# Kernel tuning notes

Hardware: AMD Instinct MI355X
Metric: run time of the kernel (lower is better)

Reference implementation:

```python
import jax, jax.numpy as jnp
import numpy as np

DIM = 192
HEADS = 6

def conv1x1(x, w):
    # x: [b,c,h,w], w: [out,in]
    return jnp.einsum('oi,bihw->bohw', w, x)

def dwconv3x3(x, w):
    # x: [b,c,h,w], w: [c,1,3,3] depthwise
    return jax.lax.conv_general_dilated(
        x, w, window_strides=(1, 1), padding='SAME',
        dimension_numbers=('NCHW', 'OIHW', 'NCHW'),
        feature_group_count=x.shape[1])

def l2norm(x, eps=1e-12):
    n = jnp.sqrt(jnp.sum(x * x, axis=-1, keepdims=True))
    return x / jnp.maximum(n, eps)

def setup_inputs() -> dict:
    key = jax.random.key(0)
    ks = jax.random.split(key, 9)
    b, c, h, w = 8, DIM, 128, 128
    s = 1.0 / np.sqrt(c)
    return {
        'x': jax.random.normal(ks[0], (b, c, h, w), jnp.float32),
        'Wq': jax.random.normal(ks[1], (c, c), jnp.float32) * s,
        'Wk': jax.random.normal(ks[2], (c, c), jnp.float32) * s,
        'Wv': jax.random.normal(ks[3], (c, c), jnp.float32) * s,
        'Wq_dw': jax.random.normal(ks[4], (c, 1, 3, 3), jnp.float32) * (1.0 / 3.0),
        'Wk_dw': jax.random.normal(ks[5], (c, 1, 3, 3), jnp.float32) * (1.0 / 3.0),
        'Wv_dw': jax.random.normal(ks[6], (c, 1, 3, 3), jnp.float32) * (1.0 / 3.0),
        'rescale': jnp.ones((HEADS, 1, 1), jnp.float32),
        'Wp': jax.random.normal(ks[7], (c, c), jnp.float32) * s,
    }

def reference(x, Wq, Wk, Wv, Wq_dw, Wk_dw, Wv_dw, rescale, Wp):
    b, c, h, w = x.shape
    hd = c // HEADS  # per-head channels
    q = dwconv3x3(conv1x1(x, Wq), Wq_dw).reshape(b, HEADS, hd, h * w)
    k = dwconv3x3(conv1x1(x, Wk), Wk_dw).reshape(b, HEADS, hd, h * w)
    v = dwconv3x3(conv1x1(x, Wv), Wv_dw).reshape(b, HEADS, hd, h * w)
    q = l2norm(q)
    k = l2norm(k)
    # attn: [b, heads, hd, hd] -- small channel-wise attention
    attn = jnp.einsum('bhcn,bhdn->bhcd', q, k) * rescale
    attn = jax.nn.softmax(attn, axis=-1)
    out = jnp.einsum('bhcd,bhdn->bhcn', attn, v).reshape(b, c, h, w)
    return conv1x1(out, Wp)
```

## Files before the change

kernel.cpp:

```cpp
#include <hip/hip_runtime.h>
#include <hip/hip_bf16.h>


using bf16x8 = __attribute__((ext_vector_type(8))) short;
using f32x4  = __attribute__((ext_vector_type(4))) float;
using fvec4  = __attribute__((ext_vector_type(4))) float;

#define NB     8
#define CDIM   192
#define NHEADS 6
#define IMGW   128
#define NPIX   16384

__device__ __forceinline__ float b2f(unsigned short u){
  return __uint_as_float(((unsigned int)u) << 16);
}
__device__ __forceinline__ unsigned short f2b(float f){
  unsigned int x = __float_as_uint(f);
  return (unsigned short)((x + 0x7FFFu + ((x >> 16) & 1u)) >> 16);
}
__device__ __forceinline__ float ldT(const void* p, size_t i, int isbf){
  return isbf ? b2f(((const unsigned short*)p)[i]) : ((const float*)p)[i];
}
__device__ __forceinline__ f32x4 MF(bf16x8 a, bf16x8 b, f32x4 c){
  return __builtin_amdgcn_mfma_f32_16x16x32_bf16(a, b, c, 0, 0, 0);
}

__global__ void k_detect(const unsigned short* x, int* flag){
  int l = threadIdx.x;
  int cnt = 0;
#pragma unroll
  for (int i = 0; i < 2; ++i){
    unsigned short u = x[(l*2 + i)*2];
    float a = fabsf(b2f(u));
    if (a == 0.f || (a > 1e-4f && a < 20.f)) ++cnt;
  }
  int tot = __popcll(__ballot(cnt >= 1)) + __popcll(__ballot(cnt >= 2));
  if (l == 0) *flag = (tot > 64) ? 1 : 0;
}

__global__ __launch_bounds__(256) void k_prep(const void* Wq, const void* Wk, const void* Wv,
    unsigned short* Wqkv, const int* flag){
  int i = blockIdx.x*256 + threadIdx.x;
  if (i >= 576*192) return;
  int isbf = *flag;
  int m = i / 192, kk = i % 192;
  int t = m / 192;
  const void* W = (t == 0) ? Wq : (t == 1) ? Wk : Wv;
  Wqkv[i] = f2b(ldT(W, (size_t)(m % 192)*192 + kk, isbf));
}

__global__ __launch_bounds__(256) void k_conv1(const void* x, const unsigned short* Wqkv,
    unsigned short* q0, unsigned short* k0, unsigned short* v0, const int* flag){
  __shared__ unsigned short Bt[64][200];
  int tid = threadIdx.x;
  int nt = blockIdx.x, b = blockIdx.y;
  int n0 = nt * 64;
  int isbf = *flag;
  if (isbf){
    const unsigned short* xs = (const unsigned short*)x;
    for (int r = tid; r < 1536; r += 256){
      int k = r >> 3, j8 = (r & 7) * 8;
      bf16x8 v = *(const bf16x8*)(xs + (size_t)(b*CDIM + k)*NPIX + n0 + j8);
#pragma unroll
      for (int i = 0; i < 8; ++i) Bt[j8+i][k] = (unsigned short)v[i];
    }
  } else {
    const float* xf = (const float*)x;
    for (int r = tid; r < 3072; r += 256){
      int k = r >> 4, j4 = (r & 15) * 4;
      fvec4 v = *(const fvec4*)(xf + (size_t)(b*CDIM + k)*NPIX + n0 + j4);
#pragma unroll
      for (int i = 0; i < 4; ++i) Bt[j4+i][k] = f2b(v[i]);
    }
  }
  __syncthreads();
  int w = tid >> 6, l = tid & 63, lr = l & 15, lk = l >> 4;
#pragma unroll 1
  for (int t = 0; t < 3; ++t){
    f32x4 acc[3][4] = {};
    for (int kc = 0; kc < 6; ++kc){
      bf16x8 af[3];
#pragma unroll
      for (int g = 0; g < 3; ++g)
        af[g] = *(const bf16x8*)(Wqkv + ((size_t)t*CDIM + g*64 + w*16 + lr)*CDIM + kc*32 + lk*8);
#pragma unroll
      for (int nf = 0; nf < 4; ++nf){
        bf16x8 bfv = *(const bf16x8*)(&Bt[nf*16 + lr][kc*32 + lk*8]);
#pragma unroll
        for (int g = 0; g < 3; ++g) acc[g][nf] = MF(af[g], bfv, acc[g][nf]);
      }
    }
    unsigned short* dst = (t == 0) ? q0 : (t == 1) ? k0 : v0;
#pragma unroll
    for (int g = 0; g < 3; ++g)
#pragma unroll
      for (int nf = 0; nf < 4; ++nf)
#pragma unroll
        for (int r = 0; r < 4; ++r){
          int m = g*64 + w*16 + lk*4 + r;
          dst[(size_t)(b*CDIM + m)*NPIX + n0 + nf*16 + lr] = f2b(acc[g][nf][r]);
        }
  }
}

__global__ __launch_bounds__(256) void k_dw(unsigned short* q0, unsigned short* k0,
    unsigned short* v0, const void* wqd, const void* wkd, const void* wvd,
    float* Nsq, const int* flag){
  __shared__ unsigned short img[128][136];
  __shared__ float wred[4];
  int tid = threadIdx.x;
  int t = blockIdx.x, c = blockIdx.y, b = blockIdx.z;
  int isbf = *flag;
  unsigned short* base = ((t == 0) ? q0 : (t == 1) ? k0 : v0) + (size_t)(b*CDIM + c)*NPIX;
  const void* wd = (t == 0) ? wqd : (t == 1) ? wkd : wvd;
  float w9[9];
#pragma unroll
  for (int e = 0; e < 9; ++e) w9[e] = ldT(wd, (size_t)c*9 + e, isbf);
  for (int r = tid; r < 2048; r += 256){
    int row = r >> 4, col8 = (r & 15)*8;
    *(bf16x8*)(&img[row][col8]) = *(const bf16x8*)(base + row*IMGW + col8);
  }
  __syncthreads();
  int tr = tid >> 2, tc = tid & 3;
  int c0 = tc * 32, r0 = tr * 2;
  const bf16x8 zv = {0,0,0,0,0,0,0,0};
  int  rowi[4]; bool valid[4];
  bf16x8 cur[4], nxt[4];
  float carry[4];
#pragma unroll
  for (int d = 0; d < 4; ++d){
    rowi[d] = r0 - 1 + d;
    valid[d] = (rowi[d] >= 0) && (rowi[d] < 128);
    cur[d] = valid[d] ? *(const bf16x8*)(&img[rowi[d]][c0]) : zv;
    carry[d] = (valid[d] && c0 > 0) ? b2f(img[rowi[d]][c0 - 1]) : 0.f;
  }
  float sq = 0.f;
#pragma unroll
  for (int j = 0; j < 4; ++j){
    float right0[4];
    if (j < 3){
#pragma unroll
      for (int d = 0; d < 4; ++d){
        nxt[d] = valid[d] ? *(const bf16x8*)(&img[rowi[d]][c0 + 8*(j+1)]) : zv;
        right0[d] = b2f((unsigned short)nxt[d][0]);
      }
    } else {
#pragma unroll
      for (int d = 0; d < 4; ++d)
        right0[d] = (valid[d] && (c0 + 32 < 128)) ? b2f(img[rowi[d]][c0 + 32]) : 0.f;
    }
    float f[4][8];
#pragma unroll
    for (int d = 0; d < 4; ++d)
#pragma unroll
      for (int i = 0; i < 8; ++i) f[d][i] = b2f((unsigned short)cur[d][i]);
#pragma unroll
    for (int rr = 0; rr < 2; ++rr){
      float o[8];
#pragma unroll
      for (int cc = 0; cc < 8; ++cc){
        float a = 0.f;
#pragma unroll
        for (int d2 = 0; d2 < 3; ++d2){
          int d = rr + d2;
          float lf = (cc == 0) ? carry[d] : f[d][cc-1];
          float md = f[d][cc];
          float rt = (cc == 7) ? right0[d] : f[d][cc+1];
          a = fmaf(w9[d2*3+0], lf, a);
          a = fmaf(w9[d2*3+1], md, a);
          a = fmaf(w9[d2*3+2], rt, a);
        }
        o[cc] = a;
        if (t < 2) sq = fmaf(a, a, sq);
      }
      bf16x8 ov;
#pragma unroll
      for (int cc = 0; cc < 8; ++cc) ov[cc] = (short)f2b(o[cc]);
      *(bf16x8*)(base + (r0 + rr)*IMGW + c0 + 8*j) = ov;
    }
#pragma unroll
    for (int d = 0; d < 4; ++d) carry[d] = f[d][7];
    if (j < 3){
#pragma unroll
      for (int d = 0; d < 4; ++d) cur[d] = nxt[d];
    }
  }
  if (t < 2){
#pragma unroll
    for (int off = 32; off > 0; off >>= 1) sq += __shfl_xor(sq, off);
    if ((tid & 63) == 0) wred[tid >> 6] = sq;
    __syncthreads();
    if (tid == 0) Nsq[((size_t)b*2 + t)*CDIM + c] = wred[0] + wred[1] + wred[2] + wred[3];
  }
}

__global__ __launch_bounds__(256) void k_gram(const unsigned short* qd,
    const unsigned short* kd, float* Spart){
  __shared__ float S_lds[1024];
  int tid = threadIdx.x;
  int cs = blockIdx.x, h = blockIdx.y, b = blockIdx.z;
  int w = tid >> 6, l = tid & 63, lr = l & 15, lk = l >> 4;
  for (int e = tid; e < 1024; e += 256) S_lds[e] = 0.f;
  __syncthreads();
  const unsigned short* qb = qd + (size_t)(b*CDIM + h*32)*NPIX;
  const unsigned short* kb = kd + (size_t)(b*CDIM + h*32)*NPIX;
  f32x4 g4[2][2] = {};
  int pxb = cs*2048 + w*512 + lk*8;
#pragma unroll
  for (int kc = 0; kc < 16; ++kc){
    int px = pxb + kc*32;
    bf16x8 a0 = *(const bf16x8*)(qb + (size_t)lr*NPIX + px);
    bf16x8 a1 = *(const bf16x8*)(qb + (size_t)(16+lr)*NPIX + px);
    bf16x8 b0 = *(const bf16x8*)(kb + (size_t)lr*NPIX + px);
    bf16x8 b1 = *(const bf16x8*)(kb + (size_t)(16+lr)*NPIX + px);
    g4[0][0] = MF(a0, b0, g4[0][0]);
    g4[0][1] = MF(a0, b1, g4[0][1]);
    g4[1][0] = MF(a1, b0, g4[1][0]);
    g4[1][1] = MF(a1, b1, g4[1][1]);
  }
  for (int wv = 0; wv < 4; ++wv){
    if (w == wv){
#pragma unroll
      for (int mi = 0; mi < 2; ++mi)
#pragma unroll
        for (int ni = 0; ni < 2; ++ni)
#pragma unroll
          for (int r = 0; r < 4; ++r)
            S_lds[(mi*16 + lk*4 + r)*32 + ni*16 + lr] += g4[mi][ni][r];
    }
    __syncthreads();
  }
  int bidx = (b*NHEADS + h)*8 + cs;
  for (int e = tid; e < 1024; e += 256) Spart[(size_t)bidx*1024 + e] = S_lds[e];
}

__global__ __launch_bounds__(256) void k_attn(const float* Spart, const float* Nsq,
    const void* rescale, float* attnG, const int* flag){
  __shared__ float S[1024];
  __shared__ float rn[64];
  int bh = blockIdx.x, tid = threadIdx.x;
  int b = bh / NHEADS, h = bh % NHEADS;
  int isbf = *flag;
  for (int e = tid; e < 1024; e += 256){
    float a = 0.f;
    for (int st = 0; st < 8; ++st) a += Spart[((size_t)bh*8 + st)*1024 + e];
    S[e] = a;
  }
  if (tid < 64){
    int t = tid >> 5, ch = h*32 + (tid & 31);
    float a = Nsq[((size_t)b*2 + t)*CDIM + ch];
    rn[tid] = 1.f / fmaxf(sqrtf(a), 1e-12f);
  }
  __syncthreads();
  if (tid < 32){
    float sc = ldT(rescale, h, isbf);
    float lo[32], mx = -1e30f;
#pragma unroll
    for (int d = 0; d < 32; ++d){
      lo[d] = S[tid*32 + d] * rn[tid] * rn[32 + d] * sc;
      mx = fmaxf(mx, lo[d]);
    }
    float sum = 0.f;
#pragma unroll
    for (int d = 0; d < 32; ++d){ lo[d] = __expf(lo[d] - mx); sum += lo[d]; }
    float inv = 1.f / sum;
#pragma unroll
    for (int d = 0; d < 32; ++d) attnG[(size_t)bh*1024 + tid*32 + d] = lo[d] * inv;
  }
}

__global__ __launch_bounds__(256) void k_mmat(const void* Wp, const float* attnG,
    unsigned short* Mb, const int* flag){
  __shared__ float at[NHEADS*1024];
  __shared__ float wp[32][200];
  int b = blockIdx.x, og = blockIdx.y, tid = threadIdx.x;
  int isbf = *flag;
  for (int e = tid; e < NHEADS*1024; e += 256) at[e] = attnG[(size_t)b*NHEADS*1024 + e];
  for (int e = tid; e < 32*192; e += 256){
    int r = e / 192, cdx = e % 192;
    wp[r][cdx] = ldT(Wp, (size_t)(og*32 + r)*CDIM + cdx, isbf);
  }
  __syncthreads();
  int r = tid >> 3, cg = tid & 7;
#pragma unroll 1
  for (int i = 0; i < 24; ++i){
    int dg = cg*24 + i;
    int hh = dg >> 5, d = dg & 31;
    float a = 0.f;
#pragma unroll
    for (int cc = 0; cc < 32; ++cc)
      a += wp[r][hh*32 + cc] * at[hh*1024 + cc*32 + d];
    Mb[(size_t)b*CDIM*CDIM + (size_t)(og*32 + r)*CDIM + dg] = f2b(a);
  }
}

__global__ __launch_bounds__(256) void k_out(const unsigned short* v, const unsigned short* Mb,
    void* out, const int* flag){
  __shared__ unsigned short Bt[64][200];
  int tid = threadIdx.x;
  int nt = blockIdx.x, b = blockIdx.y;
  int n0 = nt * 64;
  for (int r = tid; r < 1536; r += 256){
    int k = r >> 3, j8 = (r & 7) * 8;
    bf16x8 vv = *(const bf16x8*)(v + (size_t)(b*CDIM + k)*NPIX + n0 + j8);
#pragma unroll
    for (int i = 0; i < 8; ++i) Bt[j8+i][k] = (unsigned short)vv[i];
  }
  __syncthreads();
  int w = tid >> 6, l = tid & 63, lr = l & 15, lk = l >> 4;
  const unsigned short* A = Mb + (size_t)b*CDIM*CDIM;
  f32x4 acc[3][4] = {};
  for (int kc = 0; kc < 6; ++kc){
    bf16x8 af[3];
#pragma unroll
    for (int g = 0; g < 3; ++g)
      af[g] = *(const bf16x8*)(A + (size_t)(g*64 + w*16 + lr)*CDIM + kc*32 + lk*8);
#pragma unroll
    for (int nf = 0; nf < 4; ++nf){
      bf16x8 bfv = *(const bf16x8*)(&Bt[nf*16 + lr][kc*32 + lk*8]);
#pragma unroll
      for (int g = 0; g < 3; ++g) acc[g][nf] = MF(af[g], bfv, acc[g][nf]);
    }
  }
  int isbf = *flag;
#pragma unroll
  for (int g = 0; g < 3; ++g)
#pragma unroll
    for (int nf = 0; nf < 4; ++nf)
#pragma unroll
      for (int r = 0; r < 4; ++r){
        int m = g*64 + w*16 + lk*4 + r;
        size_t oi = (size_t)(b*CDIM + m)*NPIX + n0 + nf*16 + lr;
        if (isbf) ((unsigned short*)out)[oi] = f2b(acc[g][nf][r]);
        else      ((float*)out)[oi] = acc[g][nf][r];
      }
}

extern "C" void kernel_launch(void* const* d_in, const int* in_sizes, int n_in,
                              void* d_out, int out_size, void* d_ws, size_t ws_size,
                              hipStream_t stream){
  const void* x   = d_in[0];
  const void* Wq  = d_in[1];
  const void* Wk  = d_in[2];
  const void* Wv  = d_in[3];
  const void* Wqd = d_in[4];
  const void* Wkd = d_in[5];
  const void* Wvd = d_in[6];
  const void* rsc = d_in[7];
  const void* Wp  = d_in[8];

  char* ws = (char*)d_ws;
  size_t o = 0;
  int* flag             = (int*)(ws + o);            o += 256;
  unsigned short* Wqkv  = (unsigned short*)(ws + o); o += (size_t)576*192*2;
  unsigned short* q0    = (unsigned short*)(ws + o); o += (size_t)NB*CDIM*NPIX*2;
  unsigned short* k0    = (unsigned short*)(ws + o); o += (size_t)NB*CDIM*NPIX*2;
  unsigned short* v0    = (unsigned short*)(ws + o); o += (size_t)NB*CDIM*NPIX*2;
  float* Spart          = (float*)(ws + o);          o += (size_t)384*1024*4;
  float* Nsq            = (float*)(ws + o);          o += (size_t)NB*2*CDIM*4;
  float* attnG          = (float*)(ws + o);          o += (size_t)48*1024*4;
  unsigned short* Mb    = (unsigned short*)(ws + o); o += (size_t)NB*CDIM*CDIM*2;

  k_detect<<<dim3(1), 64, 0, stream>>>((const unsigned short*)x, flag);
  k_prep  <<<dim3(432), 256, 0, stream>>>(Wq, Wk, Wv, Wqkv, flag);
  k_conv1 <<<dim3(256, 8), 256, 0, stream>>>(x, Wqkv, q0, k0, v0, flag);
  k_dw    <<<dim3(3, CDIM, NB), 256, 0, stream>>>(q0, k0, v0, Wqd, Wkd, Wvd, Nsq, flag);
  k_gram  <<<dim3(8, NHEADS, NB), 256, 0, stream>>>(q0, k0, Spart);
  k_attn  <<<dim3(48), 256, 0, stream>>>(Spart, Nsq, rsc, attnG, flag);
  k_mmat  <<<dim3(NB, 6), 256, 0, stream>>>(Wp, attnG, Mb, flag);
  k_out   <<<dim3(256, 8), 256, 0, stream>>>(v0, Mb, d_out, flag);
}
```

Baseline: 280.7 us.

## Split 1x1 conv into transpose pass plus register-resident GEMM over transposed x

Adds a separate kernel that transposes x into a pixel-major bf16 buffer, so the 1x1 conv kernel can load activation fragments straight from global memory into registers with no LDS staging. Each wave keeps its 32-pixel slice in registers and loops over all 576 output channels, streaming weight fragments and writing vectorized 4-element outputs. This removes the shared-memory transpose and the scattered scalar stores. In exchange it adds a full extra read and write of x, and the transpose kernel uses strided per-channel loads with only 32x8 blocks.

```diff
diff --git a/kernel.cpp b/kernel.cpp
--- a/kernel.cpp
+++ b/kernel.cpp
@@ -5,6 +5,7 @@
 using bf16x8 = __attribute__((ext_vector_type(8))) short;
 using f32x4  = __attribute__((ext_vector_type(4))) float;
 using fvec4  = __attribute__((ext_vector_type(4))) float;
+using u16x4  = __attribute__((ext_vector_type(4))) unsigned short;
 
 #define NB     8
 #define CDIM   192
@@ -50,57 +51,72 @@
   Wqkv[i] = f2b(ldT(W, (size_t)(m % 192)*192 + kk, isbf));
 }
 
-__global__ __launch_bounds__(256) void k_conv1(const void* x, const unsigned short* Wqkv,
-    unsigned short* q0, unsigned short* k0, unsigned short* v0, const int* flag){
-  __shared__ unsigned short Bt[64][200];
+__global__ __launch_bounds__(256) void k_xT(const void* x, unsigned short* xT, const int* flag){
+  int np = blockIdx.x*256 + threadIdx.x;
+  int b = blockIdx.y;
+  int n = np*2;
+  int isbf = *flag;
+  unsigned short* dst = xT + ((size_t)b*NPIX + n)*CDIM;
+#pragma unroll 1
+  for (int cg = 0; cg < 24; ++cg){
+    bf16x8 a0, a1;
+    if (isbf){
+      const unsigned short* xs = (const unsigned short*)x + (size_t)b*CDIM*NPIX;
+#pragma unroll
+      for (int i = 0; i < 8; ++i){
+        unsigned int u = *(const unsigned int*)(xs + (size_t)(cg*8+i)*NPIX + n);
+        a0[i] = (short)(u & 0xffffu);
+        a1[i] = (short)(u >> 16);
+      }
+    } else {
+      const float* xf = (const float*)x + (size_t)b*CDIM*NPIX;
+#pragma unroll
+      for (int i = 0; i < 8; ++i){
+        fvec4 dummy;
+        float f0 = xf[(size_t)(cg*8+i)*NPIX + n];
+        float f1 = xf[(size_t)(cg*8+i)*NPIX + n + 1];
+        a0[i] = (short)f2b(f0);
+        a1[i] = (short)f2b(f1);
+        (void)dummy;
+      }
+    }
+    *(bf16x8*)(dst + cg*8)        = a0;
+    *(bf16x8*)(dst + CDIM + cg*8) = a1;
+  }
+}
+
+__global__ __launch_bounds__(256) void k_conv1t(const unsigned short* xT,
+    const unsigned short* Wqkv, unsigned short* q0, unsigned short* k0,
+    unsigned short* v0){
   int tid = threadIdx.x;
-  int nt = blockIdx.x, b = blockIdx.y;
-  int n0 = nt * 64;
-  int isbf = *flag;
-  if (isbf){
-    const unsigned short* xs = (const unsigned short*)x;
-    for (int r = tid; r < 1536; r += 256){
-      int k = r >> 3, j8 = (r & 7) * 8;
-      bf16x8 v = *(const bf16x8*)(xs + (size_t)(b*CDIM + k)*NPIX + n0 + j8);
-#pragma unroll
-      for (int i = 0; i < 8; ++i) Bt[j8+i][k] = (unsigned short)v[i];
-    }
-  } else {
-    const float* xf = (const float*)x;
-    for (int r = tid; r < 3072; r += 256){
-      int k = r >> 4, j4 = (r & 15) * 4;
-      fvec4 v = *(const fvec4*)(xf + (size_t)(b*CDIM + k)*NPIX + n0 + j4);
-#pragma unroll
-      for (int i = 0; i < 4; ++i) Bt[j4+i][k] = f2b(v[i]);
-    }
-  }
-  __syncthreads();
+  int nbk = blockIdx.x, b = blockIdx.y;
   int w = tid >> 6, l = tid & 63, lr = l & 15, lk = l >> 4;
+  int n0 = nbk*128 + w*32;
+  const unsigned short* xrow = xT + ((size_t)b*NPIX + n0)*CDIM;
+  bf16x8 afr[2][6];
+#pragma unroll
+  for (int nf = 0; nf < 2; ++nf)
+#pragma unroll
+    for (int kc = 0; kc < 6; ++kc)
+      afr[nf][kc] = *(const bf16x8*)(xrow + (size_t)(nf*16 + lr)*CDIM + kc*32 + lk*8);
 #pragma unroll 1
-  for (int t = 0; t < 3; ++t){
-    f32x4 acc[3][4] = {};
+  for (int mt = 0; mt < 36; ++mt){
+    f32x4 acc0 = {}, acc1 = {};
+#pragma unroll
     for (int kc = 0; kc < 6; ++kc){
-      bf16x8 af[3];
-#pragma unroll
-      for (int g = 0; g < 3; ++g)
-        af[g] = *(const bf16x8*)(Wqkv + ((size_t)t*CDIM + g*64 + w*16 + lr)*CDIM + kc*32 + lk*8);
-#pragma unroll
-      for (int nf = 0; nf < 4; ++nf){
-        bf16x8 bfv = *(const bf16x8*)(&Bt[nf*16 + lr][kc*32 + lk*8]);
-#pragma unroll
-        for (int g = 0; g < 3; ++g) acc[g][nf] = MF(af[g], bfv, acc[g][nf]);
-      }
-    }
-    unsigned short* dst = (t == 0) ? q0 : (t == 1) ? k0 : v0;
-#pragma unroll
-    for (int g = 0; g < 3; ++g)
-#pragma unroll
-      for (int nf = 0; nf < 4; ++nf)
-#pragma unroll
-        for (int r = 0; r < 4; ++r){
-          int m = g*64 + w*16 + lk*4 + r;
-          dst[(size_t)(b*CDIM + m)*NPIX + n0 + nf*16 + lr] = f2b(acc[g][nf][r]);
-        }
+      bf16x8 bfv = *(const bf16x8*)(Wqkv + (size_t)(mt*16 + lr)*CDIM + kc*32 + lk*8);
+      acc0 = MF(afr[0][kc], bfv, acc0);
+      acc1 = MF(afr[1][kc], bfv, acc1);
+    }
+    int t = mt / 12;
+    int mloc = (mt - t*12)*16 + lr;
+    unsigned short* dst = ((t == 0) ? q0 : (t == 1) ? k0 : v0)
+                        + (size_t)(b*CDIM + mloc)*NPIX + n0 + lk*4;
+    u16x4 p0, p1;
+#pragma unroll
+    for (int r = 0; r < 4; ++r){ p0[r] = f2b(acc0[r]); p1[r] = f2b(acc1[r]); }
+    *(u16x4*)(dst)      = p0;
+    *(u16x4*)(dst + 16) = p1;
   }
 }
 
@@ -357,6 +373,7 @@
   unsigned short* q0    = (unsigned short*)(ws + o); o += (size_t)NB*CDIM*NPIX*2;
   unsigned short* k0    = (unsigned short*)(ws + o); o += (size_t)NB*CDIM*NPIX*2;
   unsigned short* v0    = (unsigned short*)(ws + o); o += (size_t)NB*CDIM*NPIX*2;
+  unsigned short* xT    = (unsigned short*)(ws + o); o += (size_t)NB*NPIX*CDIM*2;
   float* Spart          = (float*)(ws + o);          o += (size_t)384*1024*4;
   float* Nsq            = (float*)(ws + o);          o += (size_t)NB*2*CDIM*4;
   float* attnG          = (float*)(ws + o);          o += (size_t)48*1024*4;
@@ -364,7 +381,8 @@
 
   k_detect<<<dim3(1), 64, 0, stream>>>((const unsigned short*)x, flag);
   k_prep  <<<dim3(432), 256, 0, stream>>>(Wq, Wk, Wv, Wqkv, flag);
-  k_conv1 <<<dim3(256, 8), 256, 0, stream>>>(x, Wqkv, q0, k0, v0, flag);
+  k_xT    <<<dim3(32, NB), 256, 0, stream>>>(x, xT, flag);
+  k_conv1t<<<dim3(128, NB), 256, 0, stream>>>(xT, Wqkv, q0, k0, v0);
   k_dw    <<<dim3(3, CDIM, NB), 256, 0, stream>>>(q0, k0, v0, Wqd, Wkd, Wvd, Nsq, flag);
   k_gram  <<<dim3(8, NHEADS, NB), 256, 0, stream>>>(q0, k0, Spart);
   k_attn  <<<dim3(48), 256, 0, stream>>>(Spart, Nsq, rsc, attnG, flag);
```

Measured after the change: 352.3 us. 1.26x slower.
